# Optimization experiments

Hardware: AMD Instinct MI355X
Metric: run time of the kernel (lower is better)

The kernel has to match this reference:

```python
import jax, jax.numpy as jnp
import numpy as np
import math

HEADS = 8


def rope(t):
    # t: [..., seq, dim]; lucidrains-style interleaved rotary embedding
    seq, dim = t.shape[-2], t.shape[-1]
    inv = 1.0 / (10000.0 ** (jnp.arange(0, dim, 2, dtype=jnp.float32) / dim))
    freqs = jnp.arange(seq, dtype=jnp.float32)[:, None] * inv[None, :]  # [seq, dim/2]
    freqs = jnp.repeat(freqs, 2, axis=-1)                               # [seq, dim]
    cos, sin = jnp.cos(freqs), jnp.sin(freqs)
    t2 = t.reshape(t.shape[:-1] + (dim // 2, 2))
    rot = jnp.stack([-t2[..., 1], t2[..., 0]], axis=-1).reshape(t.shape)
    return t * cos + rot * sin


def conv1x3(x, w):
    # x: [b,c,h,w], w: [out_c,in_c,1,3], padding (0,1), no bias
    return jax.lax.conv_general_dilated(
        x, w, window_strides=(1, 1), padding=((0, 0), (1, 1)),
        dimension_numbers=('NCHW', 'OIHW', 'NCHW'))


def mcl_pw(x, w_pw):
    # per-channel linear on feature axis h: w_pw [c, out_f, in_f]
    return jnp.einsum('bchw,cgh->bcgw', x, w_pw)


def setup_inputs() -> dict:
    key = jax.random.key(0)
    ks = jax.random.split(key, 10)
    b, c, f, w = 2, 8, 256, 1024
    s = 0.05
    return {
        'x': jax.random.normal(ks[0], (b, c, f, w), dtype=jnp.float32),
        'q_pw': jax.random.normal(ks[1], (c, f, f), dtype=jnp.float32) * s,
        'q_cw': jax.random.normal(ks[2], (c, c, 1, 3), dtype=jnp.float32) * s,
        'k_pw': jax.random.normal(ks[3], (c, f, f), dtype=jnp.float32) * s,
        'k_cw': jax.random.normal(ks[4], (c, c, 1, 3), dtype=jnp.float32) * s,
        'v_pw': jax.random.normal(ks[5], (c, f, f), dtype=jnp.float32) * s,
        'v_cw': jax.random.normal(ks[6], (c, c, 1, 3), dtype=jnp.float32) * s,
        'out_pw': jax.random.normal(ks[7], (c, f, f), dtype=jnp.float32) * s,
        'out_dw': jax.random.normal(ks[8], (c, c), dtype=jnp.float32) * s,
    }


def reference(x, q_pw, q_cw, k_pw, k_cw, v_pw, v_cw, out_pw, out_dw):
    b, c, h, w = x.shape
    hd = h // HEADS

    def split_heads(y):  # [b,c,h,w] -> [b,c,heads,w,hd]
        return y.transpose(0, 1, 3, 2).reshape(b, c, w, HEADS, hd).transpose(0, 1, 3, 2, 4)

    q = rope(split_heads(conv1x3(mcl_pw(x, q_pw), q_cw)))
    k = rope(split_heads(conv1x3(mcl_pw(x, k_pw), k_cw)))
    v = split_heads(conv1x3(mcl_pw(x, v_pw), v_cw))

    # non-standard scaling by sqrt(h) = sqrt(features)
    qk = jnp.einsum('bcnqd,bcnkd->bcnqk', q, k) / math.sqrt(h)
    a = jnp.einsum('bcnqk,bcnkd->bcnqd', jax.nn.softmax(qk, axis=-1), v)
    a = a.transpose(0, 1, 3, 2, 4).reshape(b, c, w, h).transpose(0, 1, 3, 2)  # [b,c,h,w]

    # out_proj: depthwise channel mix then per-channel positionwise linear
    out = jnp.einsum('bchw,dc->bdhw', a, out_dw)
    out = mcl_pw(out, out_pw)
    return out
```

## Files before the change

kernel.cpp:

```cpp
#include <hip/hip_runtime.h>
#include <hip/hip_bf16.h>

#define B 2
#define C 8
#define F 256
#define W 1024
#define NH 8
#define HD 32

typedef float f32x4 __attribute__((ext_vector_type(4)));
typedef short sh8 __attribute__((ext_vector_type(8)));
typedef short sh4 __attribute__((ext_vector_type(4)));
typedef unsigned short u16;
typedef unsigned int u32;

#define QSCALE 0.09016843880556021f

static __device__ __forceinline__ float fexp2(float x) {
#if __has_builtin(__builtin_amdgcn_exp2f)
  return __builtin_amdgcn_exp2f(x);
#else
  return __expf(x * 0.69314718056f);
#endif
}

static __device__ __forceinline__ u16 f2b(float x) {
  union { __hip_bfloat16 h; u16 u; } v;
  v.h = __float2bfloat16(x);
  return v.u;
}
static __device__ __forceinline__ sh4 pack4(float p0, float p1, float p2, float p3) {
  union { __hip_bfloat162 h2[2]; sh4 s; } u;
  u.h2[0] = __float22bfloat162_rn(make_float2(p0, p1));
  u.h2[1] = __float22bfloat162_rn(make_float2(p2, p3));
  return u.s;
}
static __device__ __forceinline__ float b2f(u16 x) {
  union { u32 u; float f; } v;
  v.u = ((u32)x) << 16;
  return v.f;
}
static __device__ __forceinline__ float ubits(u32 u) {
  union { u32 u; float f; } v;
  v.u = u;
  return v.f;
}

static __device__ __forceinline__ f32x4 mfma32(sh8 a, sh8 b, f32x4 c) {
  return __builtin_amdgcn_mfma_f32_16x16x32_bf16(a, b, c, 0, 0, 0);
}

static __device__ __forceinline__ f32x4 mfma16(sh4 a, sh4 b, f32x4 c) {
#if __has_builtin(__builtin_amdgcn_mfma_f32_16x16x16bf16_1k)
  return __builtin_amdgcn_mfma_f32_16x16x16bf16_1k(a, b, c, 0, 0, 0);
#else
  f32x4 d;
  asm("v_mfma_f32_16x16x16_bf16 %0, %1, %2, %3" : "=v"(d) : "v"(a), "v"(b), "v"(c));
  return d;
#endif
}

static __device__ __forceinline__ void gload16(const u16* g, u16* l, int ln) {
#if __has_builtin(__builtin_amdgcn_global_load_lds)
  __builtin_amdgcn_global_load_lds((const __attribute__((address_space(1))) void*)g,
                                   (__attribute__((address_space(3))) void*)l, 16, 0, 0);
#else
  *(sh8*)(l + ln * 8) = *(const sh8*)g;
#endif
}

__global__ __launch_bounds__(256) void prep(const float* __restrict__ x, u16* __restrict__ xt,
                                            const float* __restrict__ s0, const float* __restrict__ s1,
                                            const float* __restrict__ s2, const float* __restrict__ s3,
                                            u16* __restrict__ d0, u16* __restrict__ d1,
                                            u16* __restrict__ d2, u16* __restrict__ d3,
                                            float2* __restrict__ TAB) {
  const int bid = blockIdx.x;
  const int t = threadIdx.x;
  if (bid < 4096) {
    const int bc = bid >> 8, rem = bid & 255;
    const int h0 = ((rem >> 5) & 7) * 32, w0 = (rem & 31) * 32;
    __shared__ u16 sm[32][34];
    const int a = t & 31, bql = t >> 5;
    const float* src = x + ((size_t)bc * F + h0) * W + w0;
#pragma unroll
    for (int p = 0; p < 4; ++p) {
      const int hl = bql + p * 8;
      sm[a][hl] = f2b(src[(size_t)hl * W + a]);
    }
    __syncthreads();
    u16* dst = xt + ((size_t)bc * W + w0) * F + h0;
#pragma unroll
    for (int p = 0; p < 4; ++p) {
      const int wl = bql + p * 8;
      dst[(size_t)wl * F + a] = sm[wl][a];
    }
  } else if (bid < 6144) {
    const int i = bid - 4096;
    const int which = i >> 9;
    const float* s = which == 0 ? s0 : which == 1 ? s1 : which == 2 ? s2 : s3;
    u16* d = which == 0 ? d0 : which == 1 ? d1 : which == 2 ? d2 : d3;
    const int idx = (i & 511) * 256 + t;
    const float4 v = reinterpret_cast<const float4*>(s)[idx];
    union { u16 h[4]; uint2 u; } o;
    o.h[0] = f2b(v.x); o.h[1] = f2b(v.y); o.h[2] = f2b(v.z); o.h[3] = f2b(v.w);
    reinterpret_cast<uint2*>(d)[idx] = o.u;
  } else {
    const int idx = (bid - 6144) * 256 + t;
    const int j = idx >> 10, w = idx & 1023;
    const float inv = powf(10000.f, -(float)(2 * j) / 32.f);
    float sn, cs;
    sincosf((float)w * inv, &sn, &cs);
    TAB[idx] = make_float2(cs, sn);
  }
}

template <bool OUTBF>
__global__ __launch_bounds__(256) void gemm_bt(const u16* __restrict__ Aw,
                                               const u16* __restrict__ Bt,
                                               void* __restrict__ Cc) {
  const int bc = blockIdx.z;
  const int proj = blockIdx.y >> 1;
  const int g0 = (blockIdx.y & 1) * 128;
  const int w0 = blockIdx.x * 64;
  const int t = threadIdx.x;
  const int ln = t & 63, wid = t >> 6;
  const int lr = ln & 15, lk = (ln >> 4) * 8;
  const int wr = wid >> 1, wc = wid & 1;

  const u16* Ab = Aw + (size_t)proj * C * F * F + (size_t)(bc & 7) * F * F;
  const u16* Bb = Bt + (size_t)bc * W * F;

  __shared__ u16 sA[16 * 512];
  __shared__ u16 sB[8 * 512];

  const u16* ga0 = Ab + (size_t)(g0 + (wid * 2 + 0) * 16 + lr) * F + lk;
  const u16* ga1 = Ab + (size_t)(g0 + (wid * 2 + 1) * 16 + lr) * F + lk;
  const u16* gb0 = Bb + (size_t)(w0 + wid * 16 + lr) * F + lk;

  f32x4 acc[4][2] = {};

  for (int h0 = 0; h0 < F; h0 += 64) {
    __syncthreads();
    gload16(ga0 + h0,      &sA[(0 * 8 + wid * 2 + 0) * 512], ln);
    gload16(ga0 + h0 + 32, &sA[(1 * 8 + wid * 2 + 0) * 512], ln);
    gload16(ga1 + h0,      &sA[(0 * 8 + wid * 2 + 1) * 512], ln);
    gload16(ga1 + h0 + 32, &sA[(1 * 8 + wid * 2 + 1) * 512], ln);
    gload16(gb0 + h0,      &sB[(0 * 4 + wid) * 512], ln);
    gload16(gb0 + h0 + 32, &sB[(1 * 4 + wid) * 512], ln);
    __syncthreads();
#pragma unroll
    for (int kh = 0; kh < 2; ++kh) {
      sh8 af[4], bfr[2];
#pragma unroll
      for (int mi = 0; mi < 4; ++mi)
        af[mi] = *(const sh8*)&sA[((kh * 8 + wr * 4 + mi) * 64 + ln) * 8];
#pragma unroll
      for (int ni = 0; ni < 2; ++ni)
        bfr[ni] = *(const sh8*)&sB[((kh * 4 + wc * 2 + ni) * 64 + ln) * 8];
#pragma unroll
      for (int mi = 0; mi < 4; ++mi)
#pragma unroll
        for (int ni = 0; ni < 2; ++ni)
          acc[mi][ni] = mfma32(af[mi], bfr[ni], acc[mi][ni]);
    }
  }

  const int lq = ln >> 4;
  const size_t cbase = ((size_t)proj * B * C + bc) * F * W;
  if (OUTBF) {
    u16* Cb = (u16*)Cc + cbase;
#pragma unroll
    for (int mi = 0; mi < 4; ++mi)
#pragma unroll
      for (int ni = 0; ni < 2; ++ni)
#pragma unroll
        for (int r = 0; r < 4; ++r)
          Cb[(size_t)(g0 + wr * 64 + mi * 16 + lq * 4 + r) * W + w0 + wc * 32 + ni * 16 + lr] =
              f2b(acc[mi][ni][r]);
  } else {
    float* Cb = (float*)Cc + cbase;
#pragma unroll
    for (int mi = 0; mi < 4; ++mi)
#pragma unroll
      for (int ni = 0; ni < 2; ++ni)
#pragma unroll
        for (int r = 0; r < 4; ++r)
          Cb[(size_t)(g0 + wr * 64 + mi * 16 + lq * 4 + r) * W + w0 + wc * 32 + ni * 16 + lr] =
              acc[mi][ni][r];
  }
}

__global__ __launch_bounds__(256) void conv2(const u16* __restrict__ IN,
                                             const float* __restrict__ CWq,
                                             const float* __restrict__ CWk,
                                             const float* __restrict__ CWv,
                                             const float* __restrict__ TAB,
                                             u16* __restrict__ OUT) {
  const int f2 = blockIdx.x;
  const int z = blockIdx.y;
  const int proj = z >> 1, b = z & 1;
  const float* CW = proj == 0 ? CWq : proj == 1 ? CWk : CWv;
  const size_t NB = (size_t)B * C * F * W;
  const u16* INp = IN + (size_t)proj * NB;
  u16* OUTp = OUT + (size_t)proj * NB;
  const int do_rope = (proj < 2);
  const float scale = (proj == 0) ? QSCALE : 1.0f;
  const int f0 = f2 * 2;
  const int t = threadIdx.x;

  __shared__ u16 s[2][C][1040];
  __shared__ float cw[C][C][3];
  if (t < C * C * 3) ((float*)cw)[t] = CW[t];
  if (t < 16) {
    const int fi = t >> 3, c2 = t & 7;
    s[fi][c2][7] = 0;
    s[fi][c2][1032] = 0;
  }
  {
    const int l = t & 127, rsel = t >> 7;
#pragma unroll
    for (int p = 0; p < 8; ++p) {
      const int row = p * 2 + rsel;
      const int fi = row >> 3, c2 = row & 7;
      const u16* src = INp + ((size_t)(b * C + c2) * F + f0 + fi) * W + l * 8;
      *(sh8*)&s[fi][c2][8 + l * 8] = *(const sh8*)src;
    }
  }
  __syncthreads();

  float acc[2][C][4] = {};
#pragma unroll
  for (int c = 0; c < C; ++c) {
    float v[2][6];
#pragma unroll
    for (int fi = 0; fi < 2; ++fi) {
      const u32* r32 = (const u32*)&s[fi][c][0];
      const u32 r0 = r32[2 * t + 3];
      const u32 r1 = r32[2 * t + 4];
      const u32 r2 = r32[2 * t + 5];
      const u32 r3 = r32[2 * t + 6];
      v[fi][0] = ubits(r0 & 0xffff0000u);
      v[fi][1] = ubits(r1 << 16);
      v[fi][2] = ubits(r1 & 0xffff0000u);
      v[fi][3] = ubits(r2 << 16);
      v[fi][4] = ubits(r2 & 0xffff0000u);
      v[fi][5] = ubits(r3 << 16);
    }
#pragma unroll
    for (int d = 0; d < C; ++d) {
      const float c0 = cw[d][c][0], c1 = cw[d][c][1], c2_ = cw[d][c][2];
#pragma unroll
      for (int fi = 0; fi < 2; ++fi)
#pragma unroll
        for (int o = 0; o < 4; ++o)
          acc[fi][d][o] += v[fi][o] * c0 + v[fi][o + 1] * c1 + v[fi][o + 2] * c2_;
    }
  }

  float cs[4] = {1.f, 1.f, 1.f, 1.f}, sn[4] = {0.f, 0.f, 0.f, 0.f};
  if (do_rope) {
    const int j = f2 & 15;
    const float4* tp = (const float4*)(TAB + (size_t)(j * 1024 + 4 * t) * 2);
    const float4 A0 = tp[0], A1 = tp[1];
    cs[0] = A0.x; sn[0] = A0.y; cs[1] = A0.z; sn[1] = A0.w;
    cs[2] = A1.x; sn[2] = A1.y; cs[3] = A1.z; sn[3] = A1.w;
  }

#pragma unroll
  for (int d = 0; d < C; ++d) {
    sh4 pk0, pk1;
#pragma unroll
    for (int o = 0; o < 4; ++o) {
      const float a0 = acc[0][d][o], a1 = acc[1][d][o];
      float o0 = a0, o1 = a1;
      if (do_rope) { o0 = a0 * cs[o] - a1 * sn[o]; o1 = a1 * cs[o] + a0 * sn[o]; }
      pk0[o] = (short)f2b(o0 * scale);
      pk1[o] = (short)f2b(o1 * scale);
    }
    u16* dst = OUTp + ((size_t)(b * C + d) * F + f0) * W + 4 * t;
    *(sh4*)dst = pk0;
    *(sh4*)(dst + W) = pk1;
  }
}

__global__ __launch_bounds__(1024) void attn_bf(const u16* __restrict__ Q,
                                                const u16* __restrict__ K,
                                                const u16* __restrict__ Vv,
                                                u16* __restrict__ OT) {
  const int bc = blockIdx.z, n = blockIdx.y, q0 = blockIdx.x * 256;
  const int t = threadIdx.x, ln = t & 63, wid = t >> 6;
  const int lc = ln & 15, g4 = (ln >> 4) * 4;
  const int dq = (ln >> 4) * 8;
  const size_t base = ((size_t)bc * F + n * HD) * W;

  __shared__ u16 Kl[2][64 * 40];
  __shared__ u16 Vl[2][32 * 76];

  const int skey = t & 63, dp = (t >> 6) * 2;
  const u16* gK = K + base + (size_t)dp * W + skey;
  const int sd = t >> 5, kc2 = (t & 31) * 2;
  const u16* gV = Vv + base + (size_t)sd * W + kc2;

  const int qw = q0 + wid * 16 + lc;
  sh8 qf;
#pragma unroll
  for (int j = 0; j < 8; ++j) qf[j] = (short)Q[base + (size_t)(dq + j) * W + qw];

  const sh4 ones = {0x3F80, 0x3F80, 0x3F80, 0x3F80};
  f32x4 o0 = {0.f, 0.f, 0.f, 0.f}, o1 = {0.f, 0.f, 0.f, 0.f};
  f32x4 dn = {0.f, 0.f, 0.f, 0.f};

  {
    const u32 klo = gK[0], khi = gK[W];
    *(u32*)&Kl[0][skey * 40 + dp] = klo | (khi << 16);
    *(u32*)&Vl[0][sd * 76 + kc2] = *(const u32*)gV;
  }
  __syncthreads();

  for (int tile = 0; tile < 16; ++tile) {
    const int cur = tile & 1;
    u32 hvK = 0, hvV = 0;
    if (tile < 15) {
      const int off = (tile + 1) * 64;
      const u32 klo = gK[off], khi = gK[(size_t)W + off];
      hvK = klo | (khi << 16);
      hvV = *(const u32*)(gV + off);
    }

    f32x4 sf[4];
    __builtin_amdgcn_s_setprio(1);
#pragma unroll
    for (int kh = 0; kh < 4; ++kh) {
      const sh8 kf = *(const sh8*)&Kl[cur][(kh * 16 + lc) * 40 + dq];
      f32x4 z = {0.f, 0.f, 0.f, 0.f};
      sf[kh] = mfma32(kf, qf, z);
    }
    __builtin_amdgcn_s_setprio(0);

    sh4 pb[4];
#pragma unroll
    for (int kh = 0; kh < 4; ++kh) {
      const float p0 = fexp2(sf[kh][0]);
      const float p1 = fexp2(sf[kh][1]);
      const float p2 = fexp2(sf[kh][2]);
      const float p3 = fexp2(sf[kh][3]);
      pb[kh] = pack4(p0, p1, p2, p3);
    }

    __builtin_amdgcn_s_setprio(1);
#pragma unroll
    for (int kh = 0; kh < 4; ++kh) {
      const sh4 vf0 = *(const sh4*)&Vl[cur][lc * 76 + kh * 16 + g4];
      const sh4 vf1 = *(const sh4*)&Vl[cur][(16 + lc) * 76 + kh * 16 + g4];
      o0 = mfma16(pb[kh], vf0, o0);
      o1 = mfma16(pb[kh], vf1, o1);
      dn = mfma16(pb[kh], ones, dn);
    }
    __builtin_amdgcn_s_setprio(0);

    if (tile < 15) {
      *(u32*)&Kl[cur ^ 1][skey * 40 + dp] = hvK;
      *(u32*)&Vl[cur ^ 1][sd * 76 + kc2] = hvV;
    }
    __syncthreads();
  }

  const size_t obase = (size_t)bc * W * F + n * HD;
#pragma unroll
  for (int r = 0; r < 4; ++r) {
    const float inv = 1.f / dn[r];
    const int qrow = q0 + wid * 16 + g4 + r;
    OT[obase + (size_t)qrow * F + lc] = f2b(o0[r] * inv);
    OT[obase + (size_t)qrow * F + 16 + lc] = f2b(o1[r] * inv);
  }
}

__global__ __launch_bounds__(256) void chanmix2(const u16* __restrict__ A,
                                                const float* __restrict__ DW,
                                                u16* __restrict__ O1) {
  const int b = blockIdx.y;
  const int w = blockIdx.x * 4 + (threadIdx.x >> 6);
  const int f4 = (threadIdx.x & 63) * 4;
  float dwv[C][C];
#pragma unroll
  for (int d = 0; d < C; ++d)
#pragma unroll
    for (int c = 0; c < C; ++c) dwv[d][c] = DW[d * C + c];

  float av[C][4];
#pragma unroll
  for (int c = 0; c < C; ++c) {
    const uint2 raw = *(const uint2*)&A[(((size_t)(b * C + c)) * W + w) * F + f4];
    av[c][0] = ubits(raw.x << 16);
    av[c][1] = ubits(raw.x & 0xffff0000u);
    av[c][2] = ubits(raw.y << 16);
    av[c][3] = ubits(raw.y & 0xffff0000u);
  }
#pragma unroll
  for (int d = 0; d < C; ++d) {
    float s0 = 0.f, s1 = 0.f, s2 = 0.f, s3 = 0.f;
#pragma unroll
    for (int c = 0; c < C; ++c) {
      s0 += av[c][0] * dwv[d][c];
      s1 += av[c][1] * dwv[d][c];
      s2 += av[c][2] * dwv[d][c];
      s3 += av[c][3] * dwv[d][c];
    }
    *(sh4*)&O1[(((size_t)(b * C + d)) * W + w) * F + f4] = pack4(s0, s1, s2, s3);
  }
}

extern "C" void kernel_launch(void* const* d_in, const int* in_sizes, int n_in,
                              void* d_out, int out_size, void* d_ws, size_t ws_size,
                              hipStream_t stream) {
  const float* x      = (const float*)d_in[0];
  const float* q_pw   = (const float*)d_in[1];
  const float* q_cw   = (const float*)d_in[2];
  const float* k_pw   = (const float*)d_in[3];
  const float* k_cw   = (const float*)d_in[4];
  const float* v_pw   = (const float*)d_in[5];
  const float* v_cw   = (const float*)d_in[6];
  const float* out_pw = (const float*)d_in[7];
  const float* out_dw = (const float*)d_in[8];

  const size_t NB = (size_t)B * C * F * W;
  const size_t CFF = (size_t)C * F * F;

  u16* xt   = (u16*)d_ws;
  u16* wqkv = xt + NB;
  u16* wo   = wqkv + 3 * CFF;
  u16* t0b  = wo + CFF;
  u16* qkvb = t0b + 3 * NB;
  float* tab = (float*)(qkvb + 3 * NB);
  u16* obuf = t0b;
  u16* o1t  = xt;

  prep<<<4096 + 2048 + 64, 256, 0, stream>>>(
      x, xt, q_pw, k_pw, v_pw, out_pw, wqkv, wqkv + CFF, wqkv + 2 * CFF, wo, (float2*)tab);

  gemm_bt<true><<<dim3(W / 64, 6, B * C), 256, 0, stream>>>(wqkv, xt, t0b);
  conv2<<<dim3(F / 2, 3 * B), 256, 0, stream>>>(t0b, q_cw, k_cw, v_cw, tab, qkvb);

  attn_bf<<<dim3(W / 256, NH, B * C), 1024, 0, stream>>>(qkvb, qkvb + NB, qkvb + 2 * NB, obuf);

  chanmix2<<<dim3(W / 4, B), 256, 0, stream>>>(obuf, out_dw, o1t);
  gemm_bt<false><<<dim3(W / 64, 2, B * C), 256, 0, stream>>>(wo, o1t, d_out);
}
```

Measured before the change: 102.3 us.

## Double-buffer projection GEMM K-loop and store K in pair-interleaved layout

The projection GEMM now double-buffers its shared-memory A/B tiles at 32-wide k steps, prefetching the next slice while running MFMAs on the current one, with one barrier per step. The conv/rope stage writes K with adjacent feature pairs interleaved into 32-bit words, so the attention kernel loads each K pair with a single 32-bit read instead of two 16-bit reads and a shift-or. This targets global-load latency in the GEMM and load count in attention's K staging, at the cost of a more specialised K layout that couples the two kernels.

After: 99.77 us. -2.5%, faster.

```diff
diff --git a/kernel.cpp b/kernel.cpp
--- a/kernel.cpp
+++ b/kernel.cpp
@@ -34,11 +34,6 @@
   u.h2[0] = __float22bfloat162_rn(make_float2(p0, p1));
   u.h2[1] = __float22bfloat162_rn(make_float2(p2, p3));
   return u.s;
-}
-static __device__ __forceinline__ float b2f(u16 x) {
-  union { u32 u; float f; } v;
-  v.u = ((u32)x) << 16;
-  return v.f;
 }
 static __device__ __forceinline__ float ubits(u32 u) {
   union { u32 u; float f; } v;
@@ -131,8 +126,8 @@
   const u16* Ab = Aw + (size_t)proj * C * F * F + (size_t)(bc & 7) * F * F;
   const u16* Bb = Bt + (size_t)bc * W * F;
 
-  __shared__ u16 sA[16 * 512];
-  __shared__ u16 sB[8 * 512];
+  __shared__ u16 sA[2][8 * 512];
+  __shared__ u16 sB[2][4 * 512];
 
   const u16* ga0 = Ab + (size_t)(g0 + (wid * 2 + 0) * 16 + lr) * F + lk;
   const u16* ga1 = Ab + (size_t)(g0 + (wid * 2 + 1) * 16 + lr) * F + lk;
@@ -140,30 +135,32 @@
 
   f32x4 acc[4][2] = {};
 
-  for (int h0 = 0; h0 < F; h0 += 64) {
+  gload16(ga0, &sA[0][(wid * 2 + 0) * 512], ln);
+  gload16(ga1, &sA[0][(wid * 2 + 1) * 512], ln);
+  gload16(gb0, &sB[0][wid * 512], ln);
+  __syncthreads();
+
+  for (int s = 0; s < 8; ++s) {
+    const int cur = s & 1;
+    if (s < 7) {
+      const int h1 = (s + 1) * 32;
+      gload16(ga0 + h1, &sA[cur ^ 1][(wid * 2 + 0) * 512], ln);
+      gload16(ga1 + h1, &sA[cur ^ 1][(wid * 2 + 1) * 512], ln);
+      gload16(gb0 + h1, &sB[cur ^ 1][wid * 512], ln);
+    }
+    sh8 af[4], bfr[2];
+#pragma unroll
+    for (int mi = 0; mi < 4; ++mi)
+      af[mi] = *(const sh8*)&sA[cur][((wr * 4 + mi) * 64 + ln) * 8];
+#pragma unroll
+    for (int ni = 0; ni < 2; ++ni)
+      bfr[ni] = *(const sh8*)&sB[cur][((wc * 2 + ni) * 64 + ln) * 8];
+#pragma unroll
+    for (int mi = 0; mi < 4; ++mi)
+#pragma unroll
+      for (int ni = 0; ni < 2; ++ni)
+        acc[mi][ni] = mfma32(af[mi], bfr[ni], acc[mi][ni]);
     __syncthreads();
-    gload16(ga0 + h0,      &sA[(0 * 8 + wid * 2 + 0) * 512], ln);
-    gload16(ga0 + h0 + 32, &sA[(1 * 8 + wid * 2 + 0) * 512], ln);
-    gload16(ga1 + h0,      &sA[(0 * 8 + wid * 2 + 1) * 512], ln);
-    gload16(ga1 + h0 + 32, &sA[(1 * 8 + wid * 2 + 1) * 512], ln);
-    gload16(gb0 + h0,      &sB[(0 * 4 + wid) * 512], ln);
-    gload16(gb0 + h0 + 32, &sB[(1 * 4 + wid) * 512], ln);
-    __syncthreads();
-#pragma unroll
-    for (int kh = 0; kh < 2; ++kh) {
-      sh8 af[4], bfr[2];
-#pragma unroll
-      for (int mi = 0; mi < 4; ++mi)
-        af[mi] = *(const sh8*)&sA[((kh * 8 + wr * 4 + mi) * 64 + ln) * 8];
-#pragma unroll
-      for (int ni = 0; ni < 2; ++ni)
-        bfr[ni] = *(const sh8*)&sB[((kh * 4 + wc * 2 + ni) * 64 + ln) * 8];
-#pragma unroll
-      for (int mi = 0; mi < 4; ++mi)
-#pragma unroll
-        for (int ni = 0; ni < 2; ++ni)
-          acc[mi][ni] = mfma32(af[mi], bfr[ni], acc[mi][ni]);
-    }
   }
 
   const int lq = ln >> 4;
@@ -270,22 +267,30 @@
 #pragma unroll
   for (int d = 0; d < C; ++d) {
     sh4 pk0, pk1;
+    uint4 pkI;
+    u32* pkIa = (u32*)&pkI;
 #pragma unroll
     for (int o = 0; o < 4; ++o) {
       const float a0 = acc[0][d][o], a1 = acc[1][d][o];
       float o0 = a0, o1 = a1;
       if (do_rope) { o0 = a0 * cs[o] - a1 * sn[o]; o1 = a1 * cs[o] + a0 * sn[o]; }
-      pk0[o] = (short)f2b(o0 * scale);
-      pk1[o] = (short)f2b(o1 * scale);
-    }
-    u16* dst = OUTp + ((size_t)(b * C + d) * F + f0) * W + 4 * t;
-    *(sh4*)dst = pk0;
-    *(sh4*)(dst + W) = pk1;
+      const u16 e0 = f2b(o0 * scale), e1 = f2b(o1 * scale);
+      pk0[o] = (short)e0;
+      pk1[o] = (short)e1;
+      pkIa[o] = (u32)e0 | ((u32)e1 << 16);
+    }
+    if (proj == 1) {
+      *(uint4*)((u32*)OUTp + ((size_t)(b * C + d) * (F / 2) + f2) * W + 4 * t) = pkI;
+    } else {
+      u16* dst = OUTp + ((size_t)(b * C + d) * F + f0) * W + 4 * t;
+      *(sh4*)dst = pk0;
+      *(sh4*)(dst + W) = pk1;
+    }
   }
 }
 
 __global__ __launch_bounds__(1024) void attn_bf(const u16* __restrict__ Q,
-                                                const u16* __restrict__ K,
+                                                const u16* __restrict__ KI,
                                                 const u16* __restrict__ Vv,
                                                 u16* __restrict__ OT) {
   const int bc = blockIdx.z, n = blockIdx.y, q0 = blockIdx.x * 256;
@@ -298,7 +303,7 @@
   __shared__ u16 Vl[2][32 * 76];
 
   const int skey = t & 63, dp = (t >> 6) * 2;
-  const u16* gK = K + base + (size_t)dp * W + skey;
+  const u32* gK = (const u32*)KI + ((size_t)bc * (F / 2) + n * 16 + (t >> 6)) * W + skey;
   const int sd = t >> 5, kc2 = (t & 31) * 2;
   const u16* gV = Vv + base + (size_t)sd * W + kc2;
 
@@ -312,8 +317,7 @@
   f32x4 dn = {0.f, 0.f, 0.f, 0.f};
 
   {
-    const u32 klo = gK[0], khi = gK[W];
-    *(u32*)&Kl[0][skey * 40 + dp] = klo | (khi << 16);
+    *(u32*)&Kl[0][skey * 40 + dp] = gK[0];
     *(u32*)&Vl[0][sd * 76 + kc2] = *(const u32*)gV;
   }
   __syncthreads();
@@ -323,8 +327,7 @@
     u32 hvK = 0, hvV = 0;
     if (tile < 15) {
       const int off = (tile + 1) * 64;
-      const u32 klo = gK[off], khi = gK[(size_t)W + off];
-      hvK = klo | (khi << 16);
+      hvK = gK[off];
       hvV = *(const u32*)(gV + off);
     }
 
```
